# Performance work log

Hardware: AMD Instinct MI355X
Metric: run time of the kernel (lower is better)

The kernel has to match this reference:

```python
import jax, jax.numpy as jnp
import numpy as np

B, S, D, H, F = 4, 4096, 1024, 16, 4096
CAP = 0.125
ROPE_BASE = 10000.0


def setup_inputs() -> dict:
    key = jax.random.key(0)
    ks = jax.random.split(key, 9)
    scale = 0.02
    x = jax.random.normal(ks[0], (B, S, D), jnp.float32)
    causal = jnp.where(jnp.tril(jnp.ones((S, S), bool)), 0.0, -1e9).astype(jnp.float32)
    attention_mask = jnp.broadcast_to(causal[None, None], (B, 1, S, S))
    position_ids = jnp.broadcast_to(jnp.arange(S, dtype=jnp.int32), (B, S))
    return {
        "x": x,
        "attention_mask": attention_mask,
        "position_ids": position_ids,
        "router_w": jax.random.normal(ks[1], (D, 1), jnp.float32) * scale,
        "router_b": jnp.zeros((1,), jnp.float32),
        "wq": jax.random.normal(ks[2], (D, D), jnp.float32) * scale,
        "wk": jax.random.normal(ks[3], (D, D), jnp.float32) * scale,
        "wv": jax.random.normal(ks[4], (D, D), jnp.float32) * scale,
        "wo": jax.random.normal(ks[5], (D, D), jnp.float32) * scale,
        "w1": jax.random.normal(ks[6], (D, F), jnp.float32) * scale,
        "w2": jax.random.normal(ks[7], (F, D), jnp.float32) * scale,
        "ln1": jnp.ones((D,), jnp.float32),
        "ln2": jnp.ones((D,), jnp.float32),
    }


def rmsnorm(x, g):
    return x * jax.lax.rsqrt(jnp.mean(x * x, -1, keepdims=True) + 1e-6) * g


def rope(t, pos):
    # t: [b, h, n, hd], pos: [b, n]
    hd = t.shape[-1]
    inv = 1.0 / (ROPE_BASE ** (jnp.arange(0, hd, 2, dtype=jnp.float32) / hd))
    f = pos[:, None, :, None].astype(jnp.float32) * inv  # [b,1,n,hd/2]
    emb = jnp.concatenate([f, f], axis=-1)
    cos, sin = jnp.cos(emb), jnp.sin(emb)
    rot = jnp.concatenate([-t[..., hd // 2:], t[..., : hd // 2]], axis=-1)
    return t * cos + rot * sin


def reference(x, attention_mask, position_ids, router_w, router_b,
              wq, wk, wv, wo, w1, w2, ln1, ln2):
    b, s, d = x.shape
    hd = d // H
    # router
    weights = (x @ router_w)[..., 0] + router_b[0]  # [b,s]
    k = int(CAP * s)
    topv, topi = jax.lax.top_k(weights, k)
    thr = topv[:, -1]
    sel_mask = (weights > thr[:, None]).astype(x.dtype)  # selects k-1 tokens/row
    kc = k - 1
    sel_idx = jnp.sort(topi[:, :kc], axis=1)  # preserve sequence order, [b,kc]
    bidx = jnp.arange(b)[:, None]
    # gather selected tokens / positions / weights
    x_sel = x[bidx, sel_idx]                 # [b,kc,d]
    pos_sel = position_ids[bidx, sel_idx]    # [b,kc]
    w_sel = weights[bidx, sel_idx]           # [b,kc]
    m = attention_mask[:, 0]                 # [b,s,s]
    m_sel = m[bidx[:, :, None], sel_idx[:, :, None], sel_idx[:, None, :]]  # [b,kc,kc]
    # transformer block on selected tokens
    hn = rmsnorm(x_sel, ln1)

    def heads(t):
        return t.reshape(b, kc, H, hd).transpose(0, 2, 1, 3)

    q = rope(heads(hn @ wq), pos_sel)
    kk = rope(heads(hn @ wk), pos_sel)
    v = heads(hn @ wv)
    sc = jnp.einsum('bhqd,bhkd->bhqk', q, kk) / np.sqrt(hd).astype(np.float32)
    sc = sc + m_sel[:, None]
    a = jax.nn.softmax(sc, axis=-1)
    o = jnp.einsum('bhqk,bhkd->bhqd', a, v).transpose(0, 2, 1, 3).reshape(b, kc, d) @ wo
    x1 = x_sel + o
    x2 = x1 + jax.nn.gelu(rmsnorm(x1, ln2) @ w1) @ w2
    # weighted scatter back + residual passthrough for unselected tokens
    proc = x2 * w_sel[..., None]
    out = jnp.zeros_like(x).at[bidx, sel_idx].set(proc)
    return out + x * (1.0 - sel_mask)[..., None]
```

## Files before the change

kernel.cpp:

```cpp
#include <hip/hip_runtime.h>

typedef __bf16 bf16;
typedef __bf16 bf16x8 __attribute__((ext_vector_type(8)));
typedef __bf16 bf16x4 __attribute__((ext_vector_type(4)));
typedef float f32x4 __attribute__((ext_vector_type(4)));

#define B_ 4
#define S_ 4096
#define D_ 1024
#define H_ 16
#define HD_ 64
#define F_ 4096
#define KC 512
#define M_ (B_ * KC)

#define GLDS16(gp, lp)                                                        \
    __builtin_amdgcn_global_load_lds(                                         \
        (const __attribute__((address_space(1))) void*)(gp),                  \
        (__attribute__((address_space(3))) void*)(lp), 16, 0, 0)

__global__ __launch_bounds__(256) void prep_kernel(const float* __restrict__ x,
                                                   const float* __restrict__ rw,
                                                   const float* __restrict__ rb,
                                                   float* __restrict__ weights,
                                                   const float* __restrict__ wq, bf16* __restrict__ wqT,
                                                   const float* __restrict__ wk, bf16* __restrict__ wkT,
                                                   const float* __restrict__ wv, bf16* __restrict__ wvT,
                                                   const float* __restrict__ wo, bf16* __restrict__ woT,
                                                   const float* __restrict__ w1, bf16* __restrict__ w1T,
                                                   const float* __restrict__ w2, bf16* __restrict__ w2T) {
    int bid = blockIdx.x;
    if (bid < 4096) {
        int wvv = threadIdx.x >> 6, lane = threadIdx.x & 63;
        int t = bid * 4 + wvv;
        const float* xr = x + (size_t)t * D_;
        float s = 0.f;
        for (int c = 0; c < 4; c++) {
            int off = c * 256 + lane * 4;
            float4 xv = *(const float4*)(xr + off);
            float4 wv4 = *(const float4*)(rw + off);
            s += xv.x * wv4.x + xv.y * wv4.y + xv.z * wv4.z + xv.w * wv4.w;
        }
        for (int m = 32; m; m >>= 1) s += __shfl_down(s, m);
        if (lane == 0) weights[t] = s + rb[0];
        return;
    }
    bid -= 4096;
    const float* in;
    bf16* out;
    int C, R, bx, by;
    if (bid < 1024)      { in = wq; out = wqT; C = 1024; R = 1024; bx = bid & 31; by = bid >> 5; }
    else if (bid < 2048) { int t = bid - 1024; in = wk; out = wkT; C = 1024; R = 1024; bx = t & 31; by = t >> 5; }
    else if (bid < 3072) { int t = bid - 2048; in = wv; out = wvT; C = 1024; R = 1024; bx = t & 31; by = t >> 5; }
    else if (bid < 4096) { int t = bid - 3072; in = wo; out = woT; C = 1024; R = 1024; bx = t & 31; by = t >> 5; }
    else if (bid < 8192) { int t = bid - 4096; in = w1; out = w1T; C = 4096; R = 1024; bx = t & 127; by = t >> 7; }
    else                 { int t = bid - 8192; in = w2; out = w2T; C = 1024; R = 4096; bx = t & 31; by = t >> 5; }
    __shared__ bf16 tile[32][33];
    int tx = threadIdx.x & 31, ty = threadIdx.x >> 5;
    int c0 = bx * 32, r0 = by * 32;
    for (int k = 0; k < 4; k++)
        tile[ty + k * 8][tx] = (bf16)in[(size_t)(r0 + ty + k * 8) * C + c0 + tx];
    __syncthreads();
    for (int k = 0; k < 4; k++)
        out[(size_t)(c0 + ty + k * 8) * R + r0 + tx] = tile[tx][ty + k * 8];
}

__global__ __launch_bounds__(1024) void topk_kernel(const float* __restrict__ weights,
                                                    int* __restrict__ sel_idx,
                                                    float* __restrict__ w_sel,
                                                    float* __restrict__ thr,
                                                    int* __restrict__ invmap) {
    __shared__ unsigned ords[S_];
    __shared__ unsigned hist[16][256];
    __shared__ unsigned wscan[16];
    __shared__ unsigned found[2];
    int b = blockIdx.x, tid = threadIdx.x, wv = tid >> 6, lane = tid & 63;
    const float* wb = weights + (size_t)b * S_;
    for (int i = tid; i < S_; i += 1024) {
        unsigned bits = __float_as_uint(wb[i]);
        ords[i] = (bits & 0x80000000u) ? ~bits : (bits | 0x80000000u);
        invmap[b * S_ + i] = -1;
    }
    unsigned pref = 0, pmask = 0;
    int rank = 512;
    for (int level = 0; level < 4; level++) {
        int shift = 24 - level * 8;
        for (int i = tid; i < 16 * 256; i += 1024) (&hist[0][0])[i] = 0;
        __syncthreads();
        for (int i = tid; i < S_; i += 1024) {
            unsigned o = ords[i];
            if ((o & pmask) == pref) atomicAdd(&hist[wv][(o >> shift) & 255], 1u);
        }
        __syncthreads();
        unsigned val = 0, v = 0;
        if (tid < 256) {
            unsigned s = 0;
            for (int w = 0; w < 16; w++) s += hist[w][255 - tid];
            val = s;
            v = s;
            for (int d = 1; d < 64; d <<= 1) {
                unsigned u = __shfl_up(v, d);
                if (lane >= d) v += u;
            }
            if (lane == 63) wscan[wv] = v;
        }
        __syncthreads();
        if (tid < 256) {
            unsigned woff = 0;
            for (int w = 0; w < wv; w++) woff += wscan[w];
            unsigned Ccnt = v + woff;
            if (val > 0 && Ccnt >= (unsigned)rank && Ccnt - val < (unsigned)rank) {
                found[0] = 255 - (unsigned)tid;
                found[1] = Ccnt - val;
            }
        }
        __syncthreads();
        pref |= found[0] << shift;
        pmask |= 0xffu << shift;
        rank -= (int)found[1];
        __syncthreads();
    }
    unsigned T = pref;
    int need_eq = rank - 1;
    unsigned cnt = 0;
    int i0 = tid * 4;
    unsigned o4[4];
    for (int k = 0; k < 4; k++) {
        unsigned o = ords[i0 + k];
        o4[k] = o;
        cnt += (o > T) ? 1u : 0u;
        cnt += (o == T) ? 0x10000u : 0u;
    }
    unsigned v2 = cnt;
    for (int d = 1; d < 64; d <<= 1) {
        unsigned u = __shfl_up(v2, d);
        if (lane >= d) v2 += u;
    }
    if (lane == 63) wscan[wv] = v2;
    __syncthreads();
    unsigned woff2 = 0;
    for (int w = 0; w < wv; w++) woff2 += wscan[w];
    unsigned excl = woff2 + v2 - cnt;
    unsigned gbe = excl & 0xffffu, ebe = excl >> 16;
    for (int k = 0; k < 4; k++) {
        unsigned o = o4[k];
        bool gt = o > T, eq = (o == T);
        if (gt || (eq && ebe < (unsigned)need_eq)) {
            unsigned esel = (ebe < (unsigned)need_eq) ? ebe : (unsigned)need_eq;
            unsigned pos = gbe + esel;
            sel_idx[b * KC + pos] = i0 + k;
            w_sel[b * KC + pos] = wb[i0 + k];
            invmap[b * S_ + i0 + k] = (int)pos;
        }
        gbe += gt ? 1u : 0u;
        ebe += eq ? 1u : 0u;
    }
    if (tid == 0) {
        unsigned bits = (T & 0x80000000u) ? (T & 0x7fffffffu) : ~T;
        thr[b] = __uint_as_float(bits);
        sel_idx[b * KC + 511] = 0;
        w_sel[b * KC + 511] = 0.0f;
    }
}

__global__ __launch_bounds__(256) void gather_norm_kernel(const float* __restrict__ x,
                                                          const int* __restrict__ sel_idx,
                                                          const float* __restrict__ ln1,
                                                          bf16* __restrict__ hn) {
    int r = blockIdx.x, b = r >> 9, j = r & (KC - 1);
    int tid = threadIdx.x;
    bf16* outr = hn + (size_t)r * D_;
    if (j == 511) {
        ((uint2*)outr)[tid] = make_uint2(0u, 0u);
        return;
    }
    int idx = sel_idx[r];
    const float* xr = x + ((size_t)b * S_ + idx) * D_;
    float4 xv = ((const float4*)xr)[tid];
    float v[4] = {xv.x, xv.y, xv.z, xv.w}, ss = 0.f;
    for (int i = 0; i < 4; i++) ss += v[i] * v[i];
    __shared__ float red[4];
    float t = ss;
    for (int m = 32; m; m >>= 1) t += __shfl_down(t, m);
    if ((tid & 63) == 0) red[tid >> 6] = t;
    __syncthreads();
    ss = red[0] + red[1] + red[2] + red[3];
    float scale = rsqrtf(ss * (1.0f / D_) + 1e-6f);
    float4 lv = ((const float4*)ln1)[tid];
    float lg[4] = {lv.x, lv.y, lv.z, lv.w};
    bf16x4 o;
    for (int i = 0; i < 4; i++) o[i] = (bf16)(v[i] * scale * lg[i]);
    ((bf16x4*)outr)[tid] = o;
}

template <bool GELU>
__global__ __launch_bounds__(256) void gemm_bt(const bf16* __restrict__ A,
                                               const bf16* __restrict__ B0,
                                               const bf16* __restrict__ B1,
                                               const bf16* __restrict__ B2,
                                               bf16* __restrict__ C, int K, int N, int mat_shift) {
    __shared__ bf16 As[3][128 * 32];
    __shared__ bf16 Bs[3][128 * 32];
    int tid = threadIdx.x;
    int m0 = blockIdx.y * 128, n0 = blockIdx.x * 128;
    int wave = tid >> 6, lane = tid & 63, quad = lane >> 4, l16 = lane & 15;
    int wm = (wave >> 1) * 64, wn = (wave & 1) * 64;
    int mat = n0 >> mat_shift;
    const bf16* bp = (mat == 0) ? B0 : ((mat == 1) ? B1 : B2);
    int nb = n0 - (mat << mat_shift);
    int r0 = tid >> 2, ko = (tid & 3) * 8;
    const bf16* a0 = A + (size_t)(m0 + r0) * K + ko;
    const bf16* a1 = A + (size_t)(m0 + r0 + 64) * K + ko;
    const bf16* bq0 = bp + (size_t)(nb + r0) * K + ko;
    const bf16* bq1 = bp + (size_t)(nb + r0 + 64) * K + ko;
    int nk = K >> 5;
#define STAGE_T(buf, kk)                                                      \
    do {                                                                      \
        int ks = (kk) << 5;                                                   \
        GLDS16(a0 + ks, &As[buf][tid * 8]);                                   \
        GLDS16(a1 + ks, &As[buf][2048 + tid * 8]);                            \
        GLDS16(bq0 + ks, &Bs[buf][tid * 8]);                                  \
        GLDS16(bq1 + ks, &Bs[buf][2048 + tid * 8]);                           \
    } while (0)
    STAGE_T(0, 0);
    STAGE_T(1, 1);
    f32x4 acc[4][4] = {};
    int cur = 0, pf = 2;
    for (int t = 0; t < nk; t++) {
        if (t + 2 < nk) {
            STAGE_T(pf, t + 2);
            asm volatile("s_waitcnt vmcnt(8)\n\ts_barrier" ::: "memory");
        } else if (t + 1 < nk) {
            asm volatile("s_waitcnt vmcnt(4)\n\ts_barrier" ::: "memory");
        } else {
            asm volatile("s_waitcnt vmcnt(0)\n\ts_barrier" ::: "memory");
        }
        const bf16* Ac = &As[cur][0];
        const bf16* Bc = &Bs[cur][0];
        bf16x8 af[4], bfr[4];
        for (int tt = 0; tt < 4; tt++)
            af[tt] = *(const bf16x8*)(Ac + (wm + tt * 16 + l16) * 32 + quad * 8);
        for (int tt = 0; tt < 4; tt++)
            bfr[tt] = *(const bf16x8*)(Bc + (wn + tt * 16 + l16) * 32 + quad * 8);
        for (int tm = 0; tm < 4; tm++)
            for (int tn = 0; tn < 4; tn++)
                acc[tm][tn] = __builtin_amdgcn_mfma_f32_16x16x32_bf16(af[tm], bfr[tn], acc[tm][tn], 0, 0, 0);
        asm volatile("s_barrier" ::: "memory");
        cur = (cur == 2) ? 0 : cur + 1;
        pf = (pf == 2) ? 0 : pf + 1;
    }
#undef STAGE_T
    for (int tm = 0; tm < 4; tm++)
        for (int tn = 0; tn < 4; tn++) {
            int col = n0 + wn + tn * 16 + l16;
            for (int r = 0; r < 4; r++) {
                int row = m0 + wm + tm * 16 + quad * 4 + r;
                float v = acc[tm][tn][r];
                if (GELU) {
                    float x3 = v * v * v;
                    v = 0.5f * v * (1.f + tanhf(0.7978845608028654f * (v + 0.044715f * x3)));
                }
                C[(size_t)row * N + col] = (bf16)v;
            }
        }
}

__global__ __launch_bounds__(256) void rope_prep_kernel(const bf16* __restrict__ qkv,
                                                        const int* __restrict__ sel_idx,
                                                        const int* __restrict__ pos_ids,
                                                        bf16* __restrict__ Qh, bf16* __restrict__ Kh) {
    int r = blockIdx.x, b = r >> 9, j = r & (KC - 1);
    int idx = sel_idx[r];
    float pos = (j < 511) ? (float)pos_ids[b * S_ + idx] : 0.f;
    int t = threadIdx.x, h = t >> 4, tl = t & 15;
    const bf16* row = qkv + (size_t)r * 3072;
    int bh = b * H_ + h;
    size_t qbase = ((size_t)bh * KC + j) * HD_;
    for (int dd = 0; dd < 4; dd++) {
        int d = tl * 4 + dd;
        int p = (d < 32) ? d : d - 32;
        float inv = expf(-0.28782313662425572f * (float)p);
        float f = pos * inv;
        float cs = cosf(f), sn = sinf(f);
        float qd = (float)row[h * HD_ + d];
        float qo = (d < 32) ? (float)row[h * HD_ + d + 32] : (float)row[h * HD_ + d - 32];
        float qrot = (d < 32) ? -qo : qo;
        Qh[qbase + d] = (bf16)(qd * cs + qrot * sn);
        float kd = (float)row[D_ + h * HD_ + d];
        float ko = (d < 32) ? (float)row[D_ + h * HD_ + d + 32] : (float)row[D_ + h * HD_ + d - 32];
        float krot = (d < 32) ? -ko : ko;
        Kh[qbase + d] = (bf16)(kd * cs + krot * sn);
    }
}

__global__ __launch_bounds__(256) void attn_kernel(const bf16* __restrict__ Qh,
                                                   const bf16* __restrict__ Kh,
                                                   const bf16* __restrict__ qkv,
                                                   bf16* __restrict__ O) {
    __shared__ bf16 Qs[64 * 72];
    __shared__ bf16 Ks[128 * 72];
    __shared__ bf16 Vts[64 * 136];
    __shared__ bf16 Ps[64 * 136];
    int bh = blockIdx.y, qt = blockIdx.x;
    int bb = bh >> 4, hh = bh & 15;
    int q_base = qt * 64;
    int tid = threadIdx.x, wave = tid >> 6, lane = tid & 63, quad = lane >> 4, l16 = lane & 15;
    const bf16* qg = Qh + ((size_t)bh * KC + q_base) * HD_;
    for (int i = 0; i < 2; i++) {
        int c = tid * 2 + i, row = c >> 3, ko = (c & 7) * 8;
        *(uint4*)(Qs + row * 72 + ko) = *(const uint4*)(qg + row * HD_ + ko);
    }
    f32x4 oacc[4] = {};
    float mrow[4], lrow[4];
    for (int r = 0; r < 4; r++) { mrow[r] = -1e30f; lrow[r] = 0.f; }
    int kt_max = (q_base + 63) >> 7;
    for (int kt = 0; kt <= kt_max; kt++) {
        __syncthreads();
        const bf16* kg = Kh + ((size_t)bh * KC + kt * 128) * HD_;
        for (int i = 0; i < 4; i++) {
            int c = tid * 4 + i, row = c >> 3, ko = (c & 7) * 8;
            *(uint4*)(Ks + row * 72 + ko) = *(const uint4*)(kg + row * HD_ + ko);
        }
        const bf16* vbase = qkv + ((size_t)(bb * KC + kt * 128)) * 3072 + 2 * D_ + hh * HD_;
        for (int p = 0; p < 4; p++) {
            int jj = p * 32 + (tid >> 3), ko = (tid & 7) * 8;
            bf16x8 vv = *(const bf16x8*)(vbase + (size_t)jj * 3072 + ko);
            for (int e = 0; e < 8; e++) Vts[(ko + e) * 136 + jj] = vv[e];
        }
        __syncthreads();
        f32x4 sacc[8] = {};
        for (int kk = 0; kk < 2; kk++) {
            bf16x8 aq = *(const bf16x8*)(Qs + (wave * 16 + l16) * 72 + kk * 32 + quad * 8);
            for (int tn = 0; tn < 8; tn++) {
                bf16x8 bk = *(const bf16x8*)(Ks + (tn * 16 + l16) * 72 + kk * 32 + quad * 8);
                sacc[tn] = __builtin_amdgcn_mfma_f32_16x16x32_bf16(aq, bk, sacc[tn], 0, 0, 0);
            }
        }
        for (int r = 0; r < 4; r++) {
            int qi = q_base + wave * 16 + quad * 4 + r;
            float sv[8], mx = -1e30f;
            for (int tn = 0; tn < 8; tn++) {
                int kj = kt * 128 + tn * 16 + l16;
                float s = sacc[tn][r] * 0.125f;
                if (kj > qi) s = -1e30f;
                sv[tn] = s;
                mx = fmaxf(mx, s);
            }
            for (int m = 1; m < 16; m <<= 1) mx = fmaxf(mx, __shfl_xor(mx, m));
            float mnew = fmaxf(mrow[r], mx);
            float alpha = __expf(mrow[r] - mnew);
            float rs = 0.f;
            for (int tn = 0; tn < 8; tn++) {
                float pv = __expf(sv[tn] - mnew);
                rs += pv;
                Ps[(wave * 16 + quad * 4 + r) * 136 + tn * 16 + l16] = (bf16)pv;
            }
            for (int m = 1; m < 16; m <<= 1) rs += __shfl_xor(rs, m);
            lrow[r] = lrow[r] * alpha + rs;
            mrow[r] = mnew;
            for (int tn = 0; tn < 4; tn++) oacc[tn][r] *= alpha;
        }
        __syncthreads();
        for (int kk = 0; kk < 4; kk++) {
            bf16x8 ap = *(const bf16x8*)(Ps + (wave * 16 + l16) * 136 + kk * 32 + quad * 8);
            for (int tn = 0; tn < 4; tn++) {
                bf16x8 bv = *(const bf16x8*)(Vts + (tn * 16 + l16) * 136 + kk * 32 + quad * 8);
                oacc[tn] = __builtin_amdgcn_mfma_f32_16x16x32_bf16(ap, bv, oacc[tn], 0, 0, 0);
            }
        }
    }
    for (int tn = 0; tn < 4; tn++)
        for (int r = 0; r < 4; r++) {
            int rowg = bb * KC + q_base + wave * 16 + quad * 4 + r;
            int col = hh * HD_ + tn * 16 + l16;
            O[(size_t)rowg * D_ + col] = (bf16)(oacc[tn][r] / lrow[r]);
        }
}

__global__ __launch_bounds__(256) void x1norm_kernel(const float* __restrict__ x,
                                                     const bf16* __restrict__ wo_out,
                                                     const int* __restrict__ sel_idx,
                                                     const float* __restrict__ ln2,
                                                     bf16* __restrict__ h_in) {
    int r = blockIdx.x, b = r >> 9;
    int idx = sel_idx[r];
    int tid = threadIdx.x;
    const float* xr = x + ((size_t)b * S_ + idx) * D_;
    float4 xv = ((const float4*)xr)[tid];
    bf16x4 ov = ((const bf16x4*)(wo_out + (size_t)r * D_))[tid];
    float v[4] = {xv.x + (float)ov[0], xv.y + (float)ov[1], xv.z + (float)ov[2], xv.w + (float)ov[3]};
    float ss = 0.f;
    for (int i = 0; i < 4; i++) ss += v[i] * v[i];
    __shared__ float red[4];
    float t = ss;
    for (int m = 32; m; m >>= 1) t += __shfl_down(t, m);
    if ((tid & 63) == 0) red[tid >> 6] = t;
    __syncthreads();
    ss = red[0] + red[1] + red[2] + red[3];
    float scale = rsqrtf(ss * (1.0f / D_) + 1e-6f);
    float4 lv = ((const float4*)ln2)[tid];
    float lg[4] = {lv.x, lv.y, lv.z, lv.w};
    bf16x4 o;
    for (int i = 0; i < 4; i++) o[i] = (bf16)(v[i] * scale * lg[i]);
    ((bf16x4*)(h_in + (size_t)r * D_))[tid] = o;
}

__global__ __launch_bounds__(256) void out_fused_kernel(const float* __restrict__ x,
                                                        const bf16* __restrict__ wo_out,
                                                        const bf16* __restrict__ f2,
                                                        const int* __restrict__ invmap,
                                                        const float* __restrict__ weights,
                                                        const float* __restrict__ thr,
                                                        const float* __restrict__ w_sel,
                                                        float* __restrict__ out) {
    int t = blockIdx.x;
    int b = t >> 12;
    int tid = threadIdx.x;
    float w = weights[t];
    float th = thr[b];
    float4 xv = ((const float4*)(x + (size_t)t * D_))[tid];
    float4 res;
    if (w > th) { res.x = 0.f; res.y = 0.f; res.z = 0.f; res.w = 0.f; }
    else res = xv;
    int j = invmap[t];
    if (j >= 0) {
        int r = b * KC + j;
        bf16x4 wv = ((const bf16x4*)(wo_out + (size_t)r * D_))[tid];
        bf16x4 fv = ((const bf16x4*)(f2 + (size_t)r * D_))[tid];
        float ws = w_sel[r];
        res.x += ((xv.x + (float)wv[0]) + (float)fv[0]) * ws;
        res.y += ((xv.y + (float)wv[1]) + (float)fv[1]) * ws;
        res.z += ((xv.z + (float)wv[2]) + (float)fv[2]) * ws;
        res.w += ((xv.w + (float)wv[3]) + (float)fv[3]) * ws;
    }
    ((float4*)(out + (size_t)t * D_))[tid] = res;
}

extern "C" void kernel_launch(void* const* d_in, const int* in_sizes, int n_in,
                              void* d_out, int out_size, void* d_ws, size_t ws_size,
                              hipStream_t stream) {
    const float* x = (const float*)d_in[0];
    const int* pos_ids = (const int*)d_in[2];
    const float* rw = (const float*)d_in[3];
    const float* rb = (const float*)d_in[4];
    const float* wq = (const float*)d_in[5];
    const float* wk = (const float*)d_in[6];
    const float* wv = (const float*)d_in[7];
    const float* wo = (const float*)d_in[8];
    const float* w1 = (const float*)d_in[9];
    const float* w2 = (const float*)d_in[10];
    const float* ln1 = (const float*)d_in[11];
    const float* ln2 = (const float*)d_in[12];
    float* out = (float*)d_out;
    (void)in_sizes; (void)n_in; (void)out_size;

    constexpr size_t MB = 1ull << 20;
    char* scr = (ws_size >= 88 * MB) ? (char*)d_ws : (char*)d_in[1];
    float* weights = (float*)(scr + 0);
    float* thr     = (float*)(scr + 0x10000);
    int*   sel     = (int*)  (scr + 0x14000);
    float* wsel    = (float*)(scr + 0x18000);
    int*   invmap  = (int*)  (scr + 0x20000);
    bf16*  hn      = (bf16*) (scr + 1 * MB);
    bf16*  wqT     = (bf16*) (scr + 5 * MB);
    bf16*  wkT     = (bf16*) (scr + 7 * MB);
    bf16*  wvT     = (bf16*) (scr + 9 * MB);
    bf16*  qkv     = (bf16*) (scr + 11 * MB);
    bf16*  Qh      = (bf16*) (scr + 23 * MB);
    bf16*  Kh      = (bf16*) (scr + 27 * MB);
    bf16*  obuf    = (bf16*) (scr + 35 * MB);
    bf16*  woT     = (bf16*) (scr + 39 * MB);
    bf16*  wo_out  = (bf16*) (scr + 41 * MB);
    bf16*  h_in    = (bf16*) (scr + 45 * MB);
    bf16*  w1T     = (bf16*) (scr + 49 * MB);
    bf16*  h1      = (bf16*) (scr + 57 * MB);
    bf16*  w2T     = (bf16*) (scr + 73 * MB);
    bf16*  f2      = (bf16*) (scr + 81 * MB);

    prep_kernel<<<dim3(16384), 256, 0, stream>>>(x, rw, rb, weights,
                                                 wq, wqT, wk, wkT, wv, wvT,
                                                 wo, woT, w1, w1T, w2, w2T);
    topk_kernel<<<dim3(B_), 1024, 0, stream>>>(weights, sel, wsel, thr, invmap);
    gather_norm_kernel<<<dim3(M_), 256, 0, stream>>>(x, sel, ln1, hn);
    gemm_bt<false><<<dim3(24, 16), 256, 0, stream>>>(hn, wqT, wkT, wvT, qkv, D_, 3 * D_, 10);
    rope_prep_kernel<<<dim3(M_), 256, 0, stream>>>(qkv, sel, pos_ids, Qh, Kh);
    attn_kernel<<<dim3(8, B_ * H_), 256, 0, stream>>>(Qh, Kh, qkv, obuf);
    gemm_bt<false><<<dim3(8, 16), 256, 0, stream>>>(obuf, woT, woT, woT, wo_out, D_, D_, 10);
    x1norm_kernel<<<dim3(M_), 256, 0, stream>>>(x, wo_out, sel, ln2, h_in);
    gemm_bt<true><<<dim3(32, 16), 256, 0, stream>>>(h_in, w1T, w1T, w1T, h1, D_, F_, 12);
    gemm_bt<false><<<dim3(8, 16), 256, 0, stream>>>(h1, w2T, w2T, w2T, f2, F_, D_, 10);
    out_fused_kernel<<<dim3(B_ * S_), 256, 0, stream>>>(x, wo_out, f2, invmap, weights, thr, wsel, out);
}
```

Before: 612.2 us.

## Fuse RoPE into QKV GEMM, swizzle LDS, split-K the W2 GEMM

Applies RoPE inside the QKV GEMM epilogue, using positions precomputed by topk, and removes the separate rope_prep kernel and the Qh/Kh buffers. Attention now reads Q and K straight from the strided qkv buffer. The GEMM LDS layout gets an XOR swizzle to cut bank conflicts. The W2 GEMM is split-K over two z-slices that write fp32 partials, and the output kernel sums them. This trades extra fp32 partial traffic for more blocks on the small-N GEMM.

Result: no change. 600.2 us (-2.0%).

```diff
diff --git a/kernel.cpp b/kernel.cpp
--- a/kernel.cpp
+++ b/kernel.cpp
@@ -66,8 +66,10 @@
 }
 
 __global__ __launch_bounds__(1024) void topk_kernel(const float* __restrict__ weights,
+                                                    const int* __restrict__ pos_ids,
                                                     int* __restrict__ sel_idx,
                                                     float* __restrict__ w_sel,
+                                                    float* __restrict__ possel,
                                                     float* __restrict__ thr,
                                                     int* __restrict__ invmap) {
     __shared__ unsigned ords[S_];
@@ -150,6 +152,7 @@
             unsigned pos = gbe + esel;
             sel_idx[b * KC + pos] = i0 + k;
             w_sel[b * KC + pos] = wb[i0 + k];
+            possel[b * KC + pos] = (float)pos_ids[b * S_ + i0 + k];
             invmap[b * S_ + i0 + k] = (int)pos;
         }
         gbe += gt ? 1u : 0u;
@@ -160,6 +163,7 @@
         thr[b] = __uint_as_float(bits);
         sel_idx[b * KC + 511] = 0;
         w_sel[b * KC + 511] = 0.0f;
+        possel[b * KC + 511] = 0.0f;
     }
 }
 
@@ -193,26 +197,30 @@
     ((bf16x4*)outr)[tid] = o;
 }
 
-template <bool GELU>
+template <bool GELU, bool ROPE, typename OUT>
 __global__ __launch_bounds__(256) void gemm_bt(const bf16* __restrict__ A,
                                                const bf16* __restrict__ B0,
                                                const bf16* __restrict__ B1,
                                                const bf16* __restrict__ B2,
-                                               bf16* __restrict__ C, int K, int N, int mat_shift) {
+                                               OUT* __restrict__ C, int K, int lda,
+                                               int N, int mat_shift,
+                                               const float* __restrict__ possel) {
     __shared__ bf16 As[3][128 * 32];
     __shared__ bf16 Bs[3][128 * 32];
     int tid = threadIdx.x;
     int m0 = blockIdx.y * 128, n0 = blockIdx.x * 128;
+    int kz = blockIdx.z * K;
     int wave = tid >> 6, lane = tid & 63, quad = lane >> 4, l16 = lane & 15;
     int wm = (wave >> 1) * 64, wn = (wave & 1) * 64;
     int mat = n0 >> mat_shift;
     const bf16* bp = (mat == 0) ? B0 : ((mat == 1) ? B1 : B2);
     int nb = n0 - (mat << mat_shift);
-    int r0 = tid >> 2, ko = (tid & 3) * 8;
-    const bf16* a0 = A + (size_t)(m0 + r0) * K + ko;
-    const bf16* a1 = A + (size_t)(m0 + r0 + 64) * K + ko;
-    const bf16* bq0 = bp + (size_t)(nb + r0) * K + ko;
-    const bf16* bq1 = bp + (size_t)(nb + r0 + 64) * K + ko;
+    int r0 = tid >> 2;
+    int ksw = ((tid & 3) ^ ((tid >> 3) & 3)) * 8;
+    const bf16* a0 = A + (size_t)(m0 + r0) * lda + kz + ksw;
+    const bf16* a1 = A + (size_t)(m0 + r0 + 64) * lda + kz + ksw;
+    const bf16* bq0 = bp + (size_t)(nb + r0) * lda + kz + ksw;
+    const bf16* bq1 = bp + (size_t)(nb + r0 + 64) * lda + kz + ksw;
     int nk = K >> 5;
 #define STAGE_T(buf, kk)                                                      \
     do {                                                                      \
@@ -225,6 +233,7 @@
     STAGE_T(0, 0);
     STAGE_T(1, 1);
     f32x4 acc[4][4] = {};
+    int qsw = (quad ^ ((l16 >> 1) & 3)) * 8;
     int cur = 0, pf = 2;
     for (int t = 0; t < nk; t++) {
         if (t + 2 < nk) {
@@ -239,9 +248,9 @@
         const bf16* Bc = &Bs[cur][0];
         bf16x8 af[4], bfr[4];
         for (int tt = 0; tt < 4; tt++)
-            af[tt] = *(const bf16x8*)(Ac + (wm + tt * 16 + l16) * 32 + quad * 8);
+            af[tt] = *(const bf16x8*)(Ac + (wm + tt * 16 + l16) * 32 + qsw);
         for (int tt = 0; tt < 4; tt++)
-            bfr[tt] = *(const bf16x8*)(Bc + (wn + tt * 16 + l16) * 32 + quad * 8);
+            bfr[tt] = *(const bf16x8*)(Bc + (wn + tt * 16 + l16) * 32 + qsw);
         for (int tm = 0; tm < 4; tm++)
             for (int tn = 0; tn < 4; tn++)
                 acc[tm][tn] = __builtin_amdgcn_mfma_f32_16x16x32_bf16(af[tm], bfr[tn], acc[tm][tn], 0, 0, 0);
@@ -250,6 +259,28 @@
         pf = (pf == 2) ? 0 : pf + 1;
     }
 #undef STAGE_T
+    if (ROPE && n0 < 2048) {
+        float inv0 = expf(-0.28782313662425572f * (float)l16);
+        float inv1 = expf(-0.28782313662425572f * (float)(16 + l16));
+        for (int tm = 0; tm < 4; tm++)
+            for (int r = 0; r < 4; r++) {
+                int rowg = m0 + wm + tm * 16 + quad * 4 + r;
+                float pos = possel[rowg];
+                {
+                    float f = pos * inv0, cs = cosf(f), sn = sinf(f);
+                    float lo = acc[tm][0][r], hi = acc[tm][2][r];
+                    acc[tm][0][r] = lo * cs - hi * sn;
+                    acc[tm][2][r] = hi * cs + lo * sn;
+                }
+                {
+                    float f = pos * inv1, cs = cosf(f), sn = sinf(f);
+                    float lo = acc[tm][1][r], hi = acc[tm][3][r];
+                    acc[tm][1][r] = lo * cs - hi * sn;
+                    acc[tm][3][r] = hi * cs + lo * sn;
+                }
+            }
+    }
+    C += (size_t)blockIdx.z * 2048 * N;
     for (int tm = 0; tm < 4; tm++)
         for (int tn = 0; tn < 4; tn++) {
             int col = n0 + wn + tn * 16 + l16;
@@ -260,42 +291,12 @@
                     float x3 = v * v * v;
                     v = 0.5f * v * (1.f + tanhf(0.7978845608028654f * (v + 0.044715f * x3)));
                 }
-                C[(size_t)row * N + col] = (bf16)v;
-            }
-        }
-}
-
-__global__ __launch_bounds__(256) void rope_prep_kernel(const bf16* __restrict__ qkv,
-                                                        const int* __restrict__ sel_idx,
-                                                        const int* __restrict__ pos_ids,
-                                                        bf16* __restrict__ Qh, bf16* __restrict__ Kh) {
-    int r = blockIdx.x, b = r >> 9, j = r & (KC - 1);
-    int idx = sel_idx[r];
-    float pos = (j < 511) ? (float)pos_ids[b * S_ + idx] : 0.f;
-    int t = threadIdx.x, h = t >> 4, tl = t & 15;
-    const bf16* row = qkv + (size_t)r * 3072;
-    int bh = b * H_ + h;
-    size_t qbase = ((size_t)bh * KC + j) * HD_;
-    for (int dd = 0; dd < 4; dd++) {
-        int d = tl * 4 + dd;
-        int p = (d < 32) ? d : d - 32;
-        float inv = expf(-0.28782313662425572f * (float)p);
-        float f = pos * inv;
-        float cs = cosf(f), sn = sinf(f);
-        float qd = (float)row[h * HD_ + d];
-        float qo = (d < 32) ? (float)row[h * HD_ + d + 32] : (float)row[h * HD_ + d - 32];
-        float qrot = (d < 32) ? -qo : qo;
-        Qh[qbase + d] = (bf16)(qd * cs + qrot * sn);
-        float kd = (float)row[D_ + h * HD_ + d];
-        float ko = (d < 32) ? (float)row[D_ + h * HD_ + d + 32] : (float)row[D_ + h * HD_ + d - 32];
-        float krot = (d < 32) ? -ko : ko;
-        Kh[qbase + d] = (bf16)(kd * cs + krot * sn);
-    }
-}
-
-__global__ __launch_bounds__(256) void attn_kernel(const bf16* __restrict__ Qh,
-                                                   const bf16* __restrict__ Kh,
-                                                   const bf16* __restrict__ qkv,
+                C[(size_t)row * N + col] = (OUT)v;
+            }
+        }
+}
+
+__global__ __launch_bounds__(256) void attn_kernel(const bf16* __restrict__ qkv,
                                                    bf16* __restrict__ O) {
     __shared__ bf16 Qs[64 * 72];
     __shared__ bf16 Ks[128 * 72];
@@ -305,10 +306,10 @@
     int bb = bh >> 4, hh = bh & 15;
     int q_base = qt * 64;
     int tid = threadIdx.x, wave = tid >> 6, lane = tid & 63, quad = lane >> 4, l16 = lane & 15;
-    const bf16* qg = Qh + ((size_t)bh * KC + q_base) * HD_;
+    const bf16* qg = qkv + ((size_t)(bb * KC + q_base)) * 3072 + hh * HD_;
     for (int i = 0; i < 2; i++) {
         int c = tid * 2 + i, row = c >> 3, ko = (c & 7) * 8;
-        *(uint4*)(Qs + row * 72 + ko) = *(const uint4*)(qg + row * HD_ + ko);
+        *(uint4*)(Qs + row * 72 + ko) = *(const uint4*)(qg + (size_t)row * 3072 + ko);
     }
     f32x4 oacc[4] = {};
     float mrow[4], lrow[4];
@@ -316,10 +317,10 @@
     int kt_max = (q_base + 63) >> 7;
     for (int kt = 0; kt <= kt_max; kt++) {
         __syncthreads();
-        const bf16* kg = Kh + ((size_t)bh * KC + kt * 128) * HD_;
+        const bf16* kg = qkv + ((size_t)(bb * KC + kt * 128)) * 3072 + D_ + hh * HD_;
         for (int i = 0; i < 4; i++) {
             int c = tid * 4 + i, row = c >> 3, ko = (c & 7) * 8;
-            *(uint4*)(Ks + row * 72 + ko) = *(const uint4*)(kg + row * HD_ + ko);
+            *(uint4*)(Ks + row * 72 + ko) = *(const uint4*)(kg + (size_t)row * 3072 + ko);
         }
         const bf16* vbase = qkv + ((size_t)(bb * KC + kt * 128)) * 3072 + 2 * D_ + hh * HD_;
         for (int p = 0; p < 4; p++) {
@@ -407,7 +408,8 @@
 
 __global__ __launch_bounds__(256) void out_fused_kernel(const float* __restrict__ x,
                                                         const bf16* __restrict__ wo_out,
-                                                        const bf16* __restrict__ f2,
+                                                        const float* __restrict__ f2a,
+                                                        const float* __restrict__ f2b,
                                                         const int* __restrict__ invmap,
                                                         const float* __restrict__ weights,
                                                         const float* __restrict__ thr,
@@ -426,12 +428,13 @@
     if (j >= 0) {
         int r = b * KC + j;
         bf16x4 wv = ((const bf16x4*)(wo_out + (size_t)r * D_))[tid];
-        bf16x4 fv = ((const bf16x4*)(f2 + (size_t)r * D_))[tid];
+        float4 va = ((const float4*)(f2a + (size_t)r * D_))[tid];
+        float4 vb = ((const float4*)(f2b + (size_t)r * D_))[tid];
         float ws = w_sel[r];
-        res.x += ((xv.x + (float)wv[0]) + (float)fv[0]) * ws;
-        res.y += ((xv.y + (float)wv[1]) + (float)fv[1]) * ws;
-        res.z += ((xv.z + (float)wv[2]) + (float)fv[2]) * ws;
-        res.w += ((xv.w + (float)wv[3]) + (float)fv[3]) * ws;
+        res.x += ((xv.x + (float)wv[0]) + (va.x + vb.x)) * ws;
+        res.y += ((xv.y + (float)wv[1]) + (va.y + vb.y)) * ws;
+        res.z += ((xv.z + (float)wv[2]) + (va.z + vb.z)) * ws;
+        res.w += ((xv.w + (float)wv[3]) + (va.w + vb.w)) * ws;
     }
     ((float4*)(out + (size_t)t * D_))[tid] = res;
 }
@@ -460,34 +463,38 @@
     float* thr     = (float*)(scr + 0x10000);
     int*   sel     = (int*)  (scr + 0x14000);
     float* wsel    = (float*)(scr + 0x18000);
+    float* possel  = (float*)(scr + 0x1A000);
     int*   invmap  = (int*)  (scr + 0x20000);
     bf16*  hn      = (bf16*) (scr + 1 * MB);
     bf16*  wqT     = (bf16*) (scr + 5 * MB);
     bf16*  wkT     = (bf16*) (scr + 7 * MB);
     bf16*  wvT     = (bf16*) (scr + 9 * MB);
     bf16*  qkv     = (bf16*) (scr + 11 * MB);
-    bf16*  Qh      = (bf16*) (scr + 23 * MB);
-    bf16*  Kh      = (bf16*) (scr + 27 * MB);
-    bf16*  obuf    = (bf16*) (scr + 35 * MB);
-    bf16*  woT     = (bf16*) (scr + 39 * MB);
-    bf16*  wo_out  = (bf16*) (scr + 41 * MB);
-    bf16*  h_in    = (bf16*) (scr + 45 * MB);
-    bf16*  w1T     = (bf16*) (scr + 49 * MB);
-    bf16*  h1      = (bf16*) (scr + 57 * MB);
-    bf16*  w2T     = (bf16*) (scr + 73 * MB);
-    bf16*  f2      = (bf16*) (scr + 81 * MB);
+    bf16*  obuf    = (bf16*) (scr + 23 * MB);
+    bf16*  woT     = (bf16*) (scr + 27 * MB);
+    bf16*  wo_out  = (bf16*) (scr + 29 * MB);
+    bf16*  h_in    = (bf16*) (scr + 33 * MB);
+    bf16*  w1T     = (bf16*) (scr + 37 * MB);
+    bf16*  h1      = (bf16*) (scr + 45 * MB);
+    bf16*  w2T     = (bf16*) (scr + 61 * MB);
+    float* f2a     = (float*)(scr + 69 * MB);
+    float* f2b     = (float*)(scr + 77 * MB);
 
     prep_kernel<<<dim3(16384), 256, 0, stream>>>(x, rw, rb, weights,
                                                  wq, wqT, wk, wkT, wv, wvT,
                                                  wo, woT, w1, w1T, w2, w2T);
-    topk_kernel<<<dim3(B_), 1024, 0, stream>>>(weights, sel, wsel, thr, invmap);
+    topk_kernel<<<dim3(B_), 1024, 0, stream>>>(weights, pos_ids, sel, wsel, possel, thr, invmap);
     gather_norm_kernel<<<dim3(M_), 256, 0, stream>>>(x, sel, ln1, hn);
-    gemm_bt<false><<<dim3(24, 16), 256, 0, stream>>>(hn, wqT, wkT, wvT, qkv, D_, 3 * D_, 10);
-    rope_prep_kernel<<<dim3(M_), 256, 0, stream>>>(qkv, sel, pos_ids, Qh, Kh);
-    attn_kernel<<<dim3(8, B_ * H_), 256, 0, stream>>>(Qh, Kh, qkv, obuf);
-    gemm_bt<false><<<dim3(8, 16), 256, 0, stream>>>(obuf, woT, woT, woT, wo_out, D_, D_, 10);
+    gemm_bt<false, true, bf16><<<dim3(24, 16), 256, 0, stream>>>(hn, wqT, wkT, wvT, qkv,
+                                                                 1024, 1024, 3 * D_, 10, possel);
+    attn_kernel<<<dim3(8, B_ * H_), 256, 0, stream>>>(qkv, obuf);
+    gemm_bt<false, false, bf16><<<dim3(8, 16), 256, 0, stream>>>(obuf, woT, woT, woT, wo_out,
+                                                                 1024, 1024, D_, 10, nullptr);
     x1norm_kernel<<<dim3(M_), 256, 0, stream>>>(x, wo_out, sel, ln2, h_in);
-    gemm_bt<true><<<dim3(32, 16), 256, 0, stream>>>(h_in, w1T, w1T, w1T, h1, D_, F_, 12);
-    gemm_bt<false><<<dim3(8, 16), 256, 0, stream>>>(h1, w2T, w2T, w2T, f2, F_, D_, 10);
-    out_fused_kernel<<<dim3(B_ * S_), 256, 0, stream>>>(x, wo_out, f2, invmap, weights, thr, wsel, out);
-}
+    gemm_bt<true, false, bf16><<<dim3(32, 16), 256, 0, stream>>>(h_in, w1T, w1T, w1T, h1,
+                                                                 1024, 1024, F_, 12, nullptr);
+    gemm_bt<false, false, float><<<dim3(8, 16, 2), 256, 0, stream>>>(h1, w2T, w2T, w2T, f2a,
+                                                                     2048, 4096, D_, 10, nullptr);
+    out_fused_kernel<<<dim3(B_ * S_), 256, 0, stream>>>(x, wo_out, f2a, f2b, invmap,
+                                                        weights, thr, wsel, out);
+}
```
